# Optimization experiments

Measured on AMD Instinct MI355X. Metric: run time of the kernel, lower is better.

Reference implementation:

```python
import jax, jax.numpy as jnp
import numpy as np

N = 100000   # nodes
E = 3200000  # edges (avg degree 32)
D = 128      # node_input_dim
H = 32       # hidden_dim
OUT = 3


def setup_inputs() -> dict:
    key = jax.random.key(0)
    ks = jax.random.split(key, 8)
    x = jax.random.normal(ks[0], (N, D), jnp.float32)
    edge_index = jax.random.randint(ks[1], (2, E), 0, N, dtype=jnp.int32)
    W1 = jax.random.normal(ks[2], (D, H), jnp.float32) * (1.0 / np.sqrt(D))
    b1 = jnp.zeros((H,), jnp.float32)
    W2 = jax.random.normal(ks[3], (H, H), jnp.float32) * (1.0 / np.sqrt(H))
    b2 = jnp.zeros((H,), jnp.float32)
    Wfc = jax.random.normal(ks[4], (H, OUT), jnp.float32) * (1.0 / np.sqrt(H))
    bfc = jnp.zeros((OUT,), jnp.float32)
    return {"x": x, "edge_index": edge_index, "W1": W1, "b1": b1,
            "W2": W2, "b2": b2, "Wfc": Wfc, "bfc": bfc}


def gcn_conv(x, W, b, src, dst, num_nodes):
    # PyG GCNConv defaults: transform, add self-loops, symmetric deg^-1/2 norm, bias.
    h = x @ W  # [N, H]
    ones = jnp.ones(src.shape[0], x.dtype)
    # degree with self-loop (+1), counted at target index (col) as in PyG
    deg = jax.ops.segment_sum(ones, dst, num_segments=num_nodes) + 1.0
    norm = jax.lax.rsqrt(deg)  # [N]
    coef = norm[src] * norm[dst]  # [E]
    msg = h[src] * coef[:, None]  # [E, H] gather + scale
    agg = jax.ops.segment_sum(msg, dst, num_segments=num_nodes)  # scatter-add
    # self-loop contribution: norm[i]^2 * h[i]
    agg = agg + h * (norm * norm)[:, None]
    return agg + b


def reference(x, edge_index, W1, b1, W2, b2, Wfc, bfc):
    src, dst = edge_index[0], edge_index[1]
    n = x.shape[0]
    h = jax.nn.relu(gcn_conv(x, W1, b1, src, dst, n))
    h = jax.nn.relu(gcn_conv(h, W2, b2, src, dst, n))
    return jax.nn.sigmoid(h @ Wfc + bfc)
```

## Files before the change

kernel.cpp:

```cpp
#include <hip/hip_runtime.h>
#include <hip/hip_fp16.h>
#include <math.h>

#define D_IN   128
#define H_DIM  32
#define OUT_DIM 3

#define BS      512
#define LOGBS   9
#define CAP_B   17408
#define EPB_P   4096
#define NB_MAX  1024

static __device__ inline unsigned int h2u(__half2 h) {
    union { __half2 h; unsigned int u; } c; c.h = h; return c.u;
}
static __device__ inline __half2 u2h(unsigned int u) {
    union { unsigned int u; __half2 h; } c; c.u = u; return c.h;
}
static __device__ inline __half2 sh2(__half2 v, int o) {
    return u2h((unsigned int)__shfl_xor((int)h2u(v), o));
}


__global__ void k_init_cur(int* bcur, int nb) {
    int i = threadIdx.x;
    if (i < nb) bcur[i] = i * CAP_B;
}


__global__ __launch_bounds__(256) void k_part(
    const int* __restrict__ src, const int* __restrict__ dst,
    int* __restrict__ bcur, int* __restrict__ tmcsr, int e, int nb)
{
    __shared__ int hist[NB_MAX];
    __shared__ int cur[NB_MAX];
    const int t = threadIdx.x;
    for (int j = t; j < nb; j += 256) hist[j] = 0;
    __syncthreads();

    const int base = blockIdx.x * EPB_P;
    int d[EPB_P / 256], s[EPB_P / 256];
#pragma unroll
    for (int k = 0; k < EPB_P / 256; ++k) {
        int i = base + k * 256 + t;
        if (i < e) {
            d[k] = dst[i];
            s[k] = src[i];
            atomicAdd(&hist[d[k] >> LOGBS], 1);
        } else d[k] = -1;
    }
    __syncthreads();
    for (int j = t; j < nb; j += 256)
        cur[j] = hist[j] ? atomicAdd(&bcur[j], hist[j]) : 0;
    __syncthreads();
#pragma unroll
    for (int k = 0; k < EPB_P / 256; ++k) {
        if (d[k] >= 0) {
            int b = d[k] >> LOGBS;
            int pos = atomicAdd(&cur[b], 1);
            if (pos < (b + 1) * CAP_B)
                tmcsr[pos] = s[k] | ((d[k] & (BS - 1)) << 17);
        }
    }
}


__global__ __launch_bounds__(256) void k_build(
    int* __restrict__ tmcsr, const int* __restrict__ bcur,
    int* __restrict__ offs, int* __restrict__ ends, float* __restrict__ norm,
    int n)
{
    __shared__ int cnt[BS];
    __shared__ int ss[256];
    __shared__ int slice[CAP_B];

    const int t = threadIdx.x;
    const int b = blockIdx.x;
    const int base_node = b << LOGBS;
    const int bo = b * CAP_B;
    int m = bcur[b] - bo;
    if (m > CAP_B) m = CAP_B;

    cnt[t] = 0; cnt[t + 256] = 0;
    __syncthreads();

    for (int i = t; i < m; i += 256)
        atomicAdd(&cnt[tmcsr[bo + i] >> 17], 1);
    __syncthreads();

    int c0 = cnt[2 * t], c1 = cnt[2 * t + 1];
    int loc = c0 + c1;
    ss[t] = loc;
    __syncthreads();
    for (int off = 1; off < 256; off <<= 1) {
        int u = (t >= off) ? ss[t - off] : 0;
        __syncthreads();
        ss[t] += u;
        __syncthreads();
    }
    int eb = ss[t] - loc;

    int n0 = base_node + 2 * t;
    if (n0 < n) {
        offs[n0] = bo + eb;
        ends[n0] = bo + eb + c0;
        norm[n0] = rsqrtf((float)c0 + 1.0f);
    }
    if (n0 + 1 < n) {
        offs[n0 + 1] = bo + eb + c0;
        ends[n0 + 1] = bo + eb + c0 + c1;
        norm[n0 + 1] = rsqrtf((float)c1 + 1.0f);
    }
    cnt[2 * t] = eb;
    cnt[2 * t + 1] = eb + c0;
    __syncthreads();

    for (int i = t; i < m; i += 256) {
        int p = tmcsr[bo + i];
        int pos = atomicAdd(&cnt[p >> 17], 1);
        if (pos < CAP_B) slice[pos] = p & 0x1FFFF;
    }
    __syncthreads();

    for (int i = t; i < m; i += 256) tmcsr[bo + i] = slice[i];
}


__global__ __launch_bounds__(256) void k_gemm1(
    const float* __restrict__ x, const float* __restrict__ W1,
    const float* __restrict__ norm, __half* __restrict__ h1s, int n)
{
    __shared__ float Wl[D_IN * H_DIM];
    for (int i = threadIdx.x; i < D_IN * H_DIM; i += 256) Wl[i] = W1[i];
    __syncthreads();

    const int t = threadIdx.x;
    const int jg = t & 3;
    const int node = blockIdx.x * 64 + (t >> 2);
    if (node >= n) return;
    const int j0 = jg * 8;

    float acc[8];
#pragma unroll
    for (int j = 0; j < 8; ++j) acc[j] = 0.0f;

    const float* xrow = &x[(size_t)node * D_IN];
    for (int k = 0; k < D_IN; k += 4) {
        const float4 xv = *(const float4*)&xrow[k];
#pragma unroll
        for (int kk = 0; kk < 4; ++kk) {
            const float xs = (kk == 0) ? xv.x : (kk == 1) ? xv.y
                           : (kk == 2) ? xv.z : xv.w;
            const float4 wa = *(const float4*)&Wl[(k + kk) * H_DIM + j0];
            const float4 wb = *(const float4*)&Wl[(k + kk) * H_DIM + j0 + 4];
            acc[0] = fmaf(xs, wa.x, acc[0]);
            acc[1] = fmaf(xs, wa.y, acc[1]);
            acc[2] = fmaf(xs, wa.z, acc[2]);
            acc[3] = fmaf(xs, wa.w, acc[3]);
            acc[4] = fmaf(xs, wb.x, acc[4]);
            acc[5] = fmaf(xs, wb.y, acc[5]);
            acc[6] = fmaf(xs, wb.z, acc[6]);
            acc[7] = fmaf(xs, wb.w, acc[7]);
        }
    }

    const float nr = norm[node];
    uint4 pk;
    pk.x = h2u(__floats2half2_rn(acc[0]*nr, acc[1]*nr));
    pk.y = h2u(__floats2half2_rn(acc[2]*nr, acc[3]*nr));
    pk.z = h2u(__floats2half2_rn(acc[4]*nr, acc[5]*nr));
    pk.w = h2u(__floats2half2_rn(acc[6]*nr, acc[7]*nr));
    *(uint4*)&h1s[(size_t)node * H_DIM + j0] = pk;
}


__global__ __launch_bounds__(256) void k_gather_g2(
    const __half* __restrict__ hsA, const float* __restrict__ norm,
    const int* __restrict__ offs, const int* __restrict__ ends,
    const int* __restrict__ csr, const float* __restrict__ b1,
    const float* __restrict__ W2, __half* __restrict__ hsB, int n)
{
    __shared__ float Wl[H_DIM * H_DIM];
    __shared__ float bl[H_DIM];
    for (int i = threadIdx.x; i < H_DIM * H_DIM; i += 256) Wl[i] = W2[i];
    if (threadIdx.x < H_DIM) bl[threadIdx.x] = b1[threadIdx.x];
    __syncthreads();

    const int t = threadIdx.x;
    const int node = blockIdx.x * 4 + (t >> 6);
    if (node >= n) return;
    const int lane = t & 63;
    const int g = lane >> 3;
    const int q = lane & 7;

    const int beg = offs[node];
    const int end = ends[node];
    const uint2* rows = (const uint2*)hsA;

    __half2 acc0 = u2h(0u), acc1 = u2h(0u);
    int j = beg + g;
    for (; j + 8 < end; j += 16) {
        int s0 = csr[j];
        int s1 = csr[j + 8];
        uint2 r0 = rows[s0 * 8 + q];
        uint2 r1 = rows[s1 * 8 + q];
        acc0 = __hadd2(acc0, __hadd2(u2h(r0.x), u2h(r1.x)));
        acc1 = __hadd2(acc1, __hadd2(u2h(r0.y), u2h(r1.y)));
    }
    if (j < end) {
        uint2 r0 = rows[csr[j] * 8 + q];
        acc0 = __hadd2(acc0, u2h(r0.x));
        acc1 = __hadd2(acc1, u2h(r0.y));
    }
    if (g == 0) {
        uint2 r0 = rows[node * 8 + q];
        acc0 = __hadd2(acc0, u2h(r0.x));
        acc1 = __hadd2(acc1, u2h(r0.y));
    }

#pragma unroll
    for (int o = 8; o < 64; o <<= 1) {
        acc0 = __hadd2(acc0, sh2(acc0, o));
        acc1 = __hadd2(acc1, sh2(acc1, o));
    }

    const float nr = norm[node];
    float2 f0 = __half22float2(acc0);
    float2 f1 = __half22float2(acc1);
    const int kb = q * 4;
    float u0 = fmaxf(fmaf(f0.x, nr, bl[kb + 0]), 0.f);
    float u1 = fmaxf(fmaf(f0.y, nr, bl[kb + 1]), 0.f);
    float u2 = fmaxf(fmaf(f1.x, nr, bl[kb + 2]), 0.f);
    float u3 = fmaxf(fmaf(f1.y, nr, bl[kb + 3]), 0.f);

    float p[4];
#pragma unroll
    for (int jj = 0; jj < 4; ++jj) {
        int jc = 4 * g + jj;
        p[jj] = u0 * Wl[(kb + 0) * H_DIM + jc]
              + u1 * Wl[(kb + 1) * H_DIM + jc]
              + u2 * Wl[(kb + 2) * H_DIM + jc]
              + u3 * Wl[(kb + 3) * H_DIM + jc];
    }
#pragma unroll
    for (int o = 1; o < 8; o <<= 1) {
        p[0] += __shfl_xor(p[0], o); p[1] += __shfl_xor(p[1], o);
        p[2] += __shfl_xor(p[2], o); p[3] += __shfl_xor(p[3], o);
    }

    if (q == 0) {
        uint2 w;
        w.x = h2u(__floats2half2_rn(p[0] * nr, p[1] * nr));
        w.y = h2u(__floats2half2_rn(p[2] * nr, p[3] * nr));
        ((uint2*)hsB)[node * 8 + g] = w;
    }
}


__global__ __launch_bounds__(256) void k_gather_fin(
    const __half* __restrict__ hs, const float* __restrict__ norm,
    const int* __restrict__ offs, const int* __restrict__ ends,
    const int* __restrict__ csr, const float* __restrict__ b2,
    const float* __restrict__ Wfc, const float* __restrict__ bfc,
    float* __restrict__ out, int n)
{
    const int t = threadIdx.x;
    const int node = blockIdx.x * 4 + (t >> 6);
    if (node >= n) return;
    const int lane = t & 63;
    const int g = lane >> 3;
    const int q = lane & 7;

    const int beg = offs[node];
    const int end = ends[node];
    const uint2* rows = (const uint2*)hs;

    __half2 acc0 = u2h(0u), acc1 = u2h(0u);
    int j = beg + g;
    for (; j + 8 < end; j += 16) {
        int s0 = csr[j];
        int s1 = csr[j + 8];
        uint2 r0 = rows[s0 * 8 + q];
        uint2 r1 = rows[s1 * 8 + q];
        acc0 = __hadd2(acc0, __hadd2(u2h(r0.x), u2h(r1.x)));
        acc1 = __hadd2(acc1, __hadd2(u2h(r0.y), u2h(r1.y)));
    }
    if (j < end) {
        uint2 r0 = rows[csr[j] * 8 + q];
        acc0 = __hadd2(acc0, u2h(r0.x));
        acc1 = __hadd2(acc1, u2h(r0.y));
    }
    if (g == 0) {
        uint2 r0 = rows[node * 8 + q];
        acc0 = __hadd2(acc0, u2h(r0.x));
        acc1 = __hadd2(acc1, u2h(r0.y));
    }

#pragma unroll
    for (int o = 8; o < 64; o <<= 1) {
        acc0 = __hadd2(acc0, sh2(acc0, o));
        acc1 = __hadd2(acc1, sh2(acc1, o));
    }

    const float nr = norm[node];
    float2 f0 = __half22float2(acc0);
    float2 f1 = __half22float2(acc1);
    const int f = q * 4;
    float v0 = fmaxf(fmaf(f0.x, nr, b2[f + 0]), 0.f);
    float v1 = fmaxf(fmaf(f0.y, nr, b2[f + 1]), 0.f);
    float v2 = fmaxf(fmaf(f1.x, nr, b2[f + 2]), 0.f);
    float v3 = fmaxf(fmaf(f1.y, nr, b2[f + 3]), 0.f);
    float p0 = v0*Wfc[(f+0)*3+0] + v1*Wfc[(f+1)*3+0] + v2*Wfc[(f+2)*3+0] + v3*Wfc[(f+3)*3+0];
    float p1 = v0*Wfc[(f+0)*3+1] + v1*Wfc[(f+1)*3+1] + v2*Wfc[(f+2)*3+1] + v3*Wfc[(f+3)*3+1];
    float p2 = v0*Wfc[(f+0)*3+2] + v1*Wfc[(f+1)*3+2] + v2*Wfc[(f+2)*3+2] + v3*Wfc[(f+3)*3+2];
#pragma unroll
    for (int o = 1; o < 8; o <<= 1) {
        p0 += __shfl_xor(p0, o); p1 += __shfl_xor(p1, o); p2 += __shfl_xor(p2, o);
    }

    if (lane == 0) {
        out[(size_t)node * 3 + 0] = 1.0f / (1.0f + expf(-(p0 + bfc[0])));
        out[(size_t)node * 3 + 1] = 1.0f / (1.0f + expf(-(p1 + bfc[1])));
        out[(size_t)node * 3 + 2] = 1.0f / (1.0f + expf(-(p2 + bfc[2])));
    }
}


extern "C" void kernel_launch(void* const* d_in, const int* in_sizes, int n_in,
                              void* d_out, int out_size, void* d_ws, size_t ws_size,
                              hipStream_t stream)
{
    const float* x   = (const float*)d_in[0];
    const int*   ei  = (const int*)d_in[1];
    const float* W1  = (const float*)d_in[2];
    const float* b1  = (const float*)d_in[3];
    const float* W2  = (const float*)d_in[4];
    const float* b2  = (const float*)d_in[5];
    const float* Wfc = (const float*)d_in[6];
    const float* bfc = (const float*)d_in[7];
    float* out = (float*)d_out;

    const int n = in_sizes[0] / D_IN;
    const int e = in_sizes[1] / 2;
    const int* src = ei;
    const int* dst = ei + e;
    const int nb = (n + BS - 1) >> LOGBS;

    size_t nAl = ((size_t)n + 256) & ~(size_t)255;

    float* norm  = (float*)d_ws;
    int*   offs  = (int*)(norm + nAl);
    int*   ends  = offs + nAl;
    int*   bcur  = ends + nAl;
    int*   tmcsr = bcur + 256;
    __half* HbA  = (__half*)(tmcsr + (size_t)nb * CAP_B);
    __half* HbB  = HbA + nAl * H_DIM;

    const int nb_gm = (n + 63) / 64;
    const int nb_p  = (e + EPB_P - 1) / EPB_P;
    const int nb_g  = (n + 3) / 4;

    k_init_cur<<<1, 256, 0, stream>>>(bcur, nb);
    k_part <<<nb_p, 256, 0, stream>>>(src, dst, bcur, tmcsr, e, nb);
    k_build<<<nb, 256, 0, stream>>>(tmcsr, bcur, offs, ends, norm, n);

    k_gemm1<<<nb_gm, 256, 0, stream>>>(x, W1, norm, HbA, n);

    k_gather_g2<<<nb_g, 256, 0, stream>>>(HbA, norm, offs, ends, tmcsr,
                                          b1, W2, HbB, n);

    k_gather_fin<<<nb_g, 256, 0, stream>>>(HbB, norm, offs, ends, tmcsr,
                                           b2, Wfc, bfc, out, n);
}
```

Before: 225.8 us.

## Halve CSR bucket size, unroll gathers 4x, pad W2 shared tile

Halves the node-bucket size used for CSR construction, going from 512 to 256 nodes per bucket. This doubles the number of k_build blocks, gives one node per thread, and shrinks each block's shared slice, which should improve occupancy and parallelism. The gather kernels now unroll the neighbor loop to four loads in flight, hoist the self-row load, and handle the tail with a loop. The W2 tile in shared memory is padded to 33 columns to avoid bank conflicts. The trade-offs are more partition buckets with more contention on the k_part histogram, and higher register pressure in the gathers.

```diff
diff --git a/kernel.cpp b/kernel.cpp
--- a/kernel.cpp
+++ b/kernel.cpp
@@ -6,9 +6,9 @@
 #define H_DIM  32
 #define OUT_DIM 3
 
-#define BS      512
-#define LOGBS   9
-#define CAP_B   17408
+#define BS      256
+#define LOGBS   8
+#define CAP_B   9088
 #define EPB_P   4096
 #define NB_MAX  1024
 
@@ -24,7 +24,7 @@
 
 
 __global__ void k_init_cur(int* bcur, int nb) {
-    int i = threadIdx.x;
+    int i = blockIdx.x * blockDim.x + threadIdx.x;
     if (i < nb) bcur[i] = i * CAP_B;
 }
 
@@ -77,21 +77,19 @@
 
     const int t = threadIdx.x;
     const int b = blockIdx.x;
-    const int base_node = b << LOGBS;
     const int bo = b * CAP_B;
     int m = bcur[b] - bo;
     if (m > CAP_B) m = CAP_B;
 
-    cnt[t] = 0; cnt[t + 256] = 0;
+    cnt[t] = 0;
     __syncthreads();
 
     for (int i = t; i < m; i += 256)
         atomicAdd(&cnt[tmcsr[bo + i] >> 17], 1);
     __syncthreads();
 
-    int c0 = cnt[2 * t], c1 = cnt[2 * t + 1];
-    int loc = c0 + c1;
-    ss[t] = loc;
+    int c0 = cnt[t];
+    ss[t] = c0;
     __syncthreads();
     for (int off = 1; off < 256; off <<= 1) {
         int u = (t >= off) ? ss[t - off] : 0;
@@ -99,21 +97,15 @@
         ss[t] += u;
         __syncthreads();
     }
-    int eb = ss[t] - loc;
-
-    int n0 = base_node + 2 * t;
-    if (n0 < n) {
-        offs[n0] = bo + eb;
-        ends[n0] = bo + eb + c0;
-        norm[n0] = rsqrtf((float)c0 + 1.0f);
-    }
-    if (n0 + 1 < n) {
-        offs[n0 + 1] = bo + eb + c0;
-        ends[n0 + 1] = bo + eb + c0 + c1;
-        norm[n0 + 1] = rsqrtf((float)c1 + 1.0f);
-    }
-    cnt[2 * t] = eb;
-    cnt[2 * t + 1] = eb + c0;
+    int eb = ss[t] - c0;
+
+    int node = (b << LOGBS) + t;
+    if (node < n) {
+        offs[node] = bo + eb;
+        ends[node] = bo + eb + c0;
+        norm[node] = rsqrtf((float)c0 + 1.0f);
+    }
+    cnt[t] = eb;
     __syncthreads();
 
     for (int i = t; i < m; i += 256) {
@@ -181,9 +173,12 @@
     const int* __restrict__ csr, const float* __restrict__ b1,
     const float* __restrict__ W2, __half* __restrict__ hsB, int n)
 {
-    __shared__ float Wl[H_DIM * H_DIM];
+    __shared__ float Wl[H_DIM * 33];
     __shared__ float bl[H_DIM];
-    for (int i = threadIdx.x; i < H_DIM * H_DIM; i += 256) Wl[i] = W2[i];
+    for (int i = threadIdx.x; i < H_DIM * H_DIM; i += 256) {
+        int k = i >> 5, j = i & 31;
+        Wl[k * 33 + j] = W2[i];
+    }
     if (threadIdx.x < H_DIM) bl[threadIdx.x] = b1[threadIdx.x];
     __syncthreads();
 
@@ -198,25 +193,32 @@
     const int end = ends[node];
     const uint2* rows = (const uint2*)hsA;
 
+    uint2 rs = rows[node * 8 + q];
+
     __half2 acc0 = u2h(0u), acc1 = u2h(0u);
     int j = beg + g;
-    for (; j + 8 < end; j += 16) {
+    for (; j + 24 < end; j += 32) {
         int s0 = csr[j];
         int s1 = csr[j + 8];
+        int s2 = csr[j + 16];
+        int s3 = csr[j + 24];
         uint2 r0 = rows[s0 * 8 + q];
         uint2 r1 = rows[s1 * 8 + q];
-        acc0 = __hadd2(acc0, __hadd2(u2h(r0.x), u2h(r1.x)));
-        acc1 = __hadd2(acc1, __hadd2(u2h(r0.y), u2h(r1.y)));
-    }
-    if (j < end) {
+        uint2 r2 = rows[s2 * 8 + q];
+        uint2 r3 = rows[s3 * 8 + q];
+        acc0 = __hadd2(acc0, __hadd2(__hadd2(u2h(r0.x), u2h(r1.x)),
+                                     __hadd2(u2h(r2.x), u2h(r3.x))));
+        acc1 = __hadd2(acc1, __hadd2(__hadd2(u2h(r0.y), u2h(r1.y)),
+                                     __hadd2(u2h(r2.y), u2h(r3.y))));
+    }
+    for (; j < end; j += 8) {
         uint2 r0 = rows[csr[j] * 8 + q];
         acc0 = __hadd2(acc0, u2h(r0.x));
         acc1 = __hadd2(acc1, u2h(r0.y));
     }
     if (g == 0) {
-        uint2 r0 = rows[node * 8 + q];
-        acc0 = __hadd2(acc0, u2h(r0.x));
-        acc1 = __hadd2(acc1, u2h(r0.y));
+        acc0 = __hadd2(acc0, u2h(rs.x));
+        acc1 = __hadd2(acc1, u2h(rs.y));
     }
 
 #pragma unroll
@@ -238,10 +240,10 @@
 #pragma unroll
     for (int jj = 0; jj < 4; ++jj) {
         int jc = 4 * g + jj;
-        p[jj] = u0 * Wl[(kb + 0) * H_DIM + jc]
-              + u1 * Wl[(kb + 1) * H_DIM + jc]
-              + u2 * Wl[(kb + 2) * H_DIM + jc]
-              + u3 * Wl[(kb + 3) * H_DIM + jc];
+        p[jj] = u0 * Wl[(kb + 0) * 33 + jc]
+              + u1 * Wl[(kb + 1) * 33 + jc]
+              + u2 * Wl[(kb + 2) * 33 + jc]
+              + u3 * Wl[(kb + 3) * 33 + jc];
     }
 #pragma unroll
     for (int o = 1; o < 8; o <<= 1) {
@@ -276,25 +278,32 @@
     const int end = ends[node];
     const uint2* rows = (const uint2*)hs;
 
+    uint2 rs = rows[node * 8 + q];
+
     __half2 acc0 = u2h(0u), acc1 = u2h(0u);
     int j = beg + g;
-    for (; j + 8 < end; j += 16) {
+    for (; j + 24 < end; j += 32) {
         int s0 = csr[j];
         int s1 = csr[j + 8];
+        int s2 = csr[j + 16];
+        int s3 = csr[j + 24];
         uint2 r0 = rows[s0 * 8 + q];
         uint2 r1 = rows[s1 * 8 + q];
-        acc0 = __hadd2(acc0, __hadd2(u2h(r0.x), u2h(r1.x)));
-        acc1 = __hadd2(acc1, __hadd2(u2h(r0.y), u2h(r1.y)));
-    }
-    if (j < end) {
+        uint2 r2 = rows[s2 * 8 + q];
+        uint2 r3 = rows[s3 * 8 + q];
+        acc0 = __hadd2(acc0, __hadd2(__hadd2(u2h(r0.x), u2h(r1.x)),
+                                     __hadd2(u2h(r2.x), u2h(r3.x))));
+        acc1 = __hadd2(acc1, __hadd2(__hadd2(u2h(r0.y), u2h(r1.y)),
+                                     __hadd2(u2h(r2.y), u2h(r3.y))));
+    }
+    for (; j < end; j += 8) {
         uint2 r0 = rows[csr[j] * 8 + q];
         acc0 = __hadd2(acc0, u2h(r0.x));
         acc1 = __hadd2(acc1, u2h(r0.y));
     }
     if (g == 0) {
-        uint2 r0 = rows[node * 8 + q];
-        acc0 = __hadd2(acc0, u2h(r0.x));
-        acc1 = __hadd2(acc1, u2h(r0.y));
+        acc0 = __hadd2(acc0, u2h(rs.x));
+        acc1 = __hadd2(acc1, u2h(rs.y));
     }
 
 #pragma unroll
@@ -353,7 +362,7 @@
     int*   offs  = (int*)(norm + nAl);
     int*   ends  = offs + nAl;
     int*   bcur  = ends + nAl;
-    int*   tmcsr = bcur + 256;
+    int*   tmcsr = bcur + 1024;
     __half* HbA  = (__half*)(tmcsr + (size_t)nb * CAP_B);
     __half* HbB  = HbA + nAl * H_DIM;
 
@@ -361,7 +370,7 @@
     const int nb_p  = (e + EPB_P - 1) / EPB_P;
     const int nb_g  = (n + 3) / 4;
 
-    k_init_cur<<<1, 256, 0, stream>>>(bcur, nb);
+    k_init_cur<<<(nb + 255) / 256, 256, 0, stream>>>(bcur, nb);
     k_part <<<nb_p, 256, 0, stream>>>(src, dst, bcur, tmcsr, e, nb);
     k_build<<<nb, 256, 0, stream>>>(tmcsr, bcur, offs, ends, norm, n);
 
```

Result: no change. 221.5 us (-1.9%).
